# Kernel tuning notes

Hardware: AMD Instinct MI355X
Metric: run time of the kernel (lower is better)

Reference implementation:

```python
import jax, jax.numpy as jnp
import numpy as np

D = 512        # input_dim
T = 64         # n_trees
DEPTH = 3
NI = 2 ** DEPTH - 1   # 7 internal nodes
NL = 2 ** DEPTH       # 8 leaves
PPT = NI * D + NI + NL * 2   # params per tree
TOT = PPT * T + T            # + tree_weights
HID = 64


def setup_inputs() -> dict:
    key = jax.random.key(0)
    ks = jax.random.split(key, 10)
    w = lambda k, s: jax.random.normal(k, s, jnp.float32) * 0.05  # xavier-ish small gain
    return {
        "X_train": jax.random.normal(ks[0], (8192, D), jnp.float32),
        "X_test": jax.random.normal(ks[1], (32768, D), jnp.float32),
        "y_train": jax.random.randint(ks[2], (8192,), 0, 2, jnp.int64),
        "W1": w(ks[3], (HID, D)), "b1": jnp.zeros(HID), "g1": jnp.ones(HID), "be1": jnp.zeros(HID),
        "W2": w(ks[4], (HID, HID)), "b2": jnp.zeros(HID),
        "H1": w(ks[5], (2 * HID, HID)), "hb1": jnp.zeros(2 * HID),
        "g2": jnp.ones(2 * HID), "be2": jnp.zeros(2 * HID),
        "H2": w(ks[6], (2 * HID, 2 * HID)), "hb2": jnp.zeros(2 * HID),
        "H3": w(ks[7], (TOT, 2 * HID)), "hb3": jnp.zeros(TOT),
    }


def _ln(x, g, b, eps=1e-5):
    m = x.mean(-1, keepdims=True)
    v = ((x - m) ** 2).mean(-1, keepdims=True)
    return (x - m) / jnp.sqrt(v + eps) * g + b


def reference(X_train, X_test, y_train, W1, b1, g1, be1, W2, b2,
              H1, hb1, g2, be2, H2, hb2, H3, hb3):
    # --- hypernet: data encoder + param generator (Dropout is eval=identity) ---
    h = jax.nn.relu(_ln(X_train @ W1.T + b1, g1, be1))
    h = jax.nn.relu(h @ W2.T + b2)
    c = h.mean(axis=0)                              # [HID] context
    u = jax.nn.relu(_ln(c @ H1.T + hb1, g2, be2))
    u = jax.nn.relu(u @ H2.T + hb2)
    params = u @ H3.T + hb3                         # [TOT]

    # --- parse per-tree params (sequential layout) ---
    rows = params[: T * PPT].reshape(T, PPT)
    sw = rows[:, : NI * D].reshape(T, NI, D)        # split weights
    sb = rows[:, NI * D: NI * D + NI]               # split bias [T, NI]
    ll = rows[:, NI * D + NI:].reshape(T, NL, 2)    # leaf logits
    tw = params[T * PPT:]                           # tree weights [T]

    # --- soft decision trees, all trees/nodes batched ---
    # sigmoid split prob for every (sample, tree, internal node); temperature=1
    p = jax.nn.sigmoid(jnp.einsum('bd,tnd->btn', X_test, sw) + sb[None])  # [B,T,NI]
    B = X_test.shape[0]
    lp = jnp.ones((B, T, 1), X_test.dtype)
    for d in range(DEPTH):                          # unrolled fixed-depth traversal
        s = 2 ** d - 1                              # heap offset of level d
        pd = p[:, :, s: s + 2 ** d]                 # [B,T,2^d]
        lp = jnp.stack([lp * (1 - pd), lp * pd], axis=-1).reshape(B, T, 2 ** (d + 1))
    # original code adds leaf contributions twice (main loop + cleanup loop)
    lp = lp * 2.0                                   # [B,T,NL]

    leaf_dist = jax.nn.softmax(ll, axis=-1)         # [T,NL,2]
    out_t = jnp.einsum('btl,tlc->btc', lp, leaf_dist)
    w = jax.nn.softmax(tw, axis=0)                  # [T]
    return jnp.einsum('btc,t->bc', out_t, w)        # [B,2]
```

## Files before the change

kernel.cpp:

```cpp
#include <hip/hip_runtime.h>
#include <hip/hip_bf16.h>

#define DD 512
#define HIDN 64
#define NTREE 64
#define NIN 7
#define PPTC 3607
#define TOTP 230912
#define SWROWS 448

typedef __attribute__((ext_vector_type(8))) short bf16x8;
typedef __attribute__((ext_vector_type(4))) float f32x4;
typedef __attribute__((ext_vector_type(8))) _Float16 h16x8;

__device__ __forceinline__ unsigned short f2bf(float f) {
  unsigned u = __float_as_uint(f);
  unsigned r = (u + 0x7FFFu + ((u >> 16) & 1u)) >> 16;
  return (unsigned short)r;
}
__device__ __forceinline__ float sigmoidf_(float x) {
  return 1.0f / (1.0f + __expf(-x));
}
__device__ __forceinline__ uint2 pack_bf16x4(float4 v) {
  uint2 pk;
  pk.x = (unsigned)f2bf(v.x) | ((unsigned)f2bf(v.y) << 16);
  pk.y = (unsigned)f2bf(v.z) | ((unsigned)f2bf(v.w) << 16);
  return pk;
}
__device__ __forceinline__ bf16x8 cvt8(float4 a, float4 b) {
  unsigned u0, u1, u2, u3;
  asm("v_cvt_pk_bf16_f32 %0, %1, %2" : "=v"(u0) : "v"(a.x), "v"(a.y));
  asm("v_cvt_pk_bf16_f32 %0, %1, %2" : "=v"(u1) : "v"(a.z), "v"(a.w));
  asm("v_cvt_pk_bf16_f32 %0, %1, %2" : "=v"(u2) : "v"(b.x), "v"(b.y));
  asm("v_cvt_pk_bf16_f32 %0, %1, %2" : "=v"(u3) : "v"(b.z), "v"(b.w));
  union { unsigned u[4]; bf16x8 v; } r;
  r.u[0] = u0; r.u[1] = u1; r.u[2] = u2; r.u[3] = u3;
  return r.v;
}
__device__ __forceinline__ void gl_lds16(const void* g, void* l) {
  __builtin_amdgcn_global_load_lds(
      (const __attribute__((address_space(1))) unsigned int*)g,
      (__attribute__((address_space(3))) unsigned int*)l, 16, 0, 0);
}

__global__ __launch_bounds__(256) void k_train(
    const float* __restrict__ Xtr, const float* __restrict__ W1,
    const float* __restrict__ b1, const float* __restrict__ g1,
    const float* __restrict__ be1, const float* __restrict__ W2,
    const float* __restrict__ b2, float* __restrict__ c_part)
{
  __shared__ __align__(16) char smem[37888];
  char* Xc  = smem;
  char* W1c = smem + 8192;
  char* Hl  = smem + 24576;
  char* W2l = smem + 28672;
  float* lnb = (float*)(smem + 36864);
  float* cp  = (float*)(smem + 37376);

  const int tid = threadIdx.x;
  const int lane = tid & 63;
  const int wv = tid >> 6;
  const int l15 = lane & 15;
  const int gq = lane >> 4;
  const int wm = wv >> 1;
  const int wn = wv & 1;
  const int rb0 = blockIdx.x * 32;

  const float4* X4g = (const float4*)Xtr;
  const float4* W4g = (const float4*)W1;

#pragma unroll
  for (int s = 0; s < 4; ++s) {
    int fidx = tid + s * 256;
    int n = fidx >> 4, kq = fidx & 15;
    float4 v = ((const float4*)W2)[n * 16 + kq];
    uint2 pk = pack_bf16x4(v);
    int off = n * 128 + kq * 8; off ^= (n & 7) << 4;
    *(uint2*)(W2l + off) = pk;
  }

  int xga[4], xo[4];
#pragma unroll
  for (int s = 0; s < 4; ++s) {
    int f = tid + s * 256;
    int m = f >> 5, kq = f & 31;
    xga[s] = (rb0 + m) * 128 + kq;
    xo[s] = (m * 256 + kq * 8) ^ ((m & 7) << 4);
  }
  int wga[8], wo[8];
#pragma unroll
  for (int s = 0; s < 8; ++s) {
    int f = tid + s * 256;
    int n = f >> 5, kq = f & 31;
    wga[s] = n * 128 + kq;
    wo[s] = (n * 256 + kq * 8) ^ ((n & 7) << 4);
  }

  f32x4 acc1[2];
#pragma unroll
  for (int nt = 0; nt < 2; ++nt) { f32x4 z = {0.f,0.f,0.f,0.f}; acc1[nt] = z; }

  float4 xr[4], wr[8];
#pragma unroll
  for (int s = 0; s < 4; ++s) xr[s] = X4g[xga[s]];
#pragma unroll
  for (int s = 0; s < 8; ++s) wr[s] = W4g[wga[s]];

  for (int kc = 0; kc < 4; ++kc) {
    __syncthreads();
#pragma unroll
    for (int s = 0; s < 4; ++s) *(uint2*)(Xc + xo[s]) = pack_bf16x4(xr[s]);
#pragma unroll
    for (int s = 0; s < 8; ++s) *(uint2*)(W1c + wo[s]) = pack_bf16x4(wr[s]);
    if (kc < 3) {
      int ko = (kc + 1) * 32;
#pragma unroll
      for (int s = 0; s < 4; ++s) xr[s] = X4g[xga[s] + ko];
#pragma unroll
      for (int s = 0; s < 8; ++s) wr[s] = W4g[wga[s] + ko];
    }
    __syncthreads();
#pragma unroll
    for (int ks = 0; ks < 4; ++ks) {
      int arow = wm * 16 + l15;
      int aoff = (arow * 256 + ks * 64 + gq * 16) ^ ((arow & 7) << 4);
      bf16x8 afr = *(const bf16x8*)(Xc + aoff);
#pragma unroll
      for (int nt = 0; nt < 2; ++nt) {
        int brow = wn * 32 + nt * 16 + l15;
        int boff = (brow * 256 + ks * 64 + gq * 16) ^ ((brow & 7) << 4);
        bf16x8 bfr = *(const bf16x8*)(W1c + boff);
        acc1[nt] = __builtin_amdgcn_mfma_f32_16x16x32_bf16(afr, bfr, acc1[nt], 0, 0, 0);
      }
    }
  }

  float b1v[2], g1v[2], be1v[2], b2v[2];
#pragma unroll
  for (int nt = 0; nt < 2; ++nt) {
    int c = wn * 32 + nt * 16 + l15;
    b1v[nt] = b1[c]; g1v[nt] = g1[c]; be1v[nt] = be1[c]; b2v[nt] = b2[c];
  }
  float yv[2][4], s_[4], q_[4];
#pragma unroll
  for (int i = 0; i < 4; ++i) {
    float s = 0.f, q = 0.f;
#pragma unroll
    for (int nt = 0; nt < 2; ++nt) {
      float y = acc1[nt][i] + b1v[nt];
      yv[nt][i] = y; s += y; q += y * y;
    }
    s_[i] = s; q_[i] = q;
  }
#pragma unroll
  for (int off = 1; off < 16; off <<= 1) {
#pragma unroll
    for (int i = 0; i < 4; ++i) {
      s_[i] += __shfl_xor(s_[i], off);
      q_[i] += __shfl_xor(q_[i], off);
    }
  }
  if (l15 == 0) {
#pragma unroll
    for (int i = 0; i < 4; ++i) {
      int row = wm * 16 + gq * 4 + i;
      float2 sv; sv.x = s_[i]; sv.y = q_[i];
      *(float2*)(lnb + (row * 2 + wn) * 2) = sv;
    }
  }
  __syncthreads();
#pragma unroll
  for (int i = 0; i < 4; ++i) {
    int row = wm * 16 + gq * 4 + i;
    float2 e0 = *(float2*)(lnb + (row * 2 + 0) * 2);
    float2 e1 = *(float2*)(lnb + (row * 2 + 1) * 2);
    float m = (e0.x + e1.x) * (1.0f / 64.0f);
    float var = (e0.y + e1.y) * (1.0f / 64.0f) - m * m;
    float rstd = rsqrtf(var + 1e-5f);
#pragma unroll
    for (int nt = 0; nt < 2; ++nt) {
      float h = (yv[nt][i] - m) * rstd * g1v[nt] + be1v[nt];
      h = fmaxf(h, 0.0f);
      int col = wn * 32 + nt * 16 + l15;
      int off2 = (row * 128 + col * 2) ^ ((row & 7) << 4);
      *(unsigned short*)(Hl + off2) = f2bf(h);
    }
  }
  __syncthreads();

  f32x4 acc2[2];
#pragma unroll
  for (int nt = 0; nt < 2; ++nt) { f32x4 z = {0.f,0.f,0.f,0.f}; acc2[nt] = z; }
#pragma unroll
  for (int ks = 0; ks < 2; ++ks) {
    int arow = wm * 16 + l15;
    int aoff = (arow * 128 + ks * 64 + gq * 16) ^ ((arow & 7) << 4);
    bf16x8 afr = *(const bf16x8*)(Hl + aoff);
#pragma unroll
    for (int nt = 0; nt < 2; ++nt) {
      int brow = wn * 32 + nt * 16 + l15;
      int boff = (brow * 128 + ks * 64 + gq * 16) ^ ((brow & 7) << 4);
      bf16x8 bfr = *(const bf16x8*)(W2l + boff);
      acc2[nt] = __builtin_amdgcn_mfma_f32_16x16x32_bf16(afr, bfr, acc2[nt], 0, 0, 0);
    }
  }
  float cs[2];
#pragma unroll
  for (int nt = 0; nt < 2; ++nt) {
    float s = 0.f;
#pragma unroll
    for (int i = 0; i < 4; ++i) s += fmaxf(acc2[nt][i] + b2v[nt], 0.0f);
    cs[nt] = s;
  }
#pragma unroll
  for (int nt = 0; nt < 2; ++nt) {
    cs[nt] += __shfl_xor(cs[nt], 16);
    cs[nt] += __shfl_xor(cs[nt], 32);
  }
  if (lane < 16) {
#pragma unroll
    for (int nt = 0; nt < 2; ++nt)
      cp[wm * 64 + wn * 32 + nt * 16 + lane] = cs[nt];
  }
  __syncthreads();
  if (tid < 64) c_part[blockIdx.x * 64 + tid] = cp[tid] + cp[64 + tid];
}

__global__ __launch_bounds__(256) void k_head(
    const float* __restrict__ c_part,
    const float* __restrict__ H1, const float* __restrict__ hb1,
    const float* __restrict__ g2, const float* __restrict__ be2,
    const float* __restrict__ H2, const float* __restrict__ hb2,
    float* __restrict__ u2out)
{
  __shared__ float part[256];
  __shared__ float clds[64];
  __shared__ float u1lds[128];
  __shared__ float red[8];
  int tid = threadIdx.x;
  {
    int col = tid & 63, g = tid >> 6;
    float s0 = 0.f, s1 = 0.f, s2 = 0.f, s3 = 0.f;
    int b0 = g * 64;
    for (int b = 0; b < 64; b += 4) {
      s0 += c_part[(b0 + b + 0) * 64 + col];
      s1 += c_part[(b0 + b + 1) * 64 + col];
      s2 += c_part[(b0 + b + 2) * 64 + col];
      s3 += c_part[(b0 + b + 3) * 64 + col];
    }
    part[tid] = (s0 + s1) + (s2 + s3);
  }
  __syncthreads();
  if (tid < 64)
    clds[tid] = (part[tid] + part[64 + tid] + part[128 + tid] + part[192 + tid]) * (1.0f / 8192.0f);
  __syncthreads();
  float acc = 0.f;
  if (tid < 128) {
    float a0 = 0.f, a1 = 0.f, a2 = 0.f, a3 = 0.f;
    for (int k = 0; k < 64; k += 4) {
      a0 += clds[k + 0] * H1[tid * 64 + k + 0];
      a1 += clds[k + 1] * H1[tid * 64 + k + 1];
      a2 += clds[k + 2] * H1[tid * 64 + k + 2];
      a3 += clds[k + 3] * H1[tid * 64 + k + 3];
    }
    acc = hb1[tid] + ((a0 + a1) + (a2 + a3));
  }
  float s = acc, q = acc * acc;
#pragma unroll
  for (int off = 1; off < 64; off <<= 1) { s += __shfl_xor(s, off); q += __shfl_xor(q, off); }
  int wv = tid >> 6;
  if ((tid & 63) == 0) { red[wv * 2] = s; red[wv * 2 + 1] = q; }
  __syncthreads();
  float S = red[0] + red[2], Q = red[1] + red[3];
  float m = S * (1.0f / 128.0f);
  float var = Q * (1.0f / 128.0f) - m * m;
  float rstd = rsqrtf(var + 1e-5f);
  if (tid < 128)
    u1lds[tid] = fmaxf((acc - m) * rstd * g2[tid] + be2[tid], 0.0f);
  __syncthreads();
  if (tid < 128) {
    float c0 = 0.f, c1 = 0.f, c2 = 0.f, c3 = 0.f;
    for (int k = 0; k < 128; k += 4) {
      c0 += u1lds[k + 0] * H2[tid * 128 + k + 0];
      c1 += u1lds[k + 1] * H2[tid * 128 + k + 1];
      c2 += u1lds[k + 2] * H2[tid * 128 + k + 2];
      c3 += u1lds[k + 3] * H2[tid * 128 + k + 3];
    }
    u2out[tid] = fmaxf(hb2[tid] + ((c0 + c1) + (c2 + c3)), 0.0f);
  }
}

__global__ __launch_bounds__(256) void k_params(
    const float* __restrict__ H3, const float* __restrict__ hb3,
    const float* __restrict__ u2,
    unsigned short* __restrict__ Bsw, float* __restrict__ sb,
    float* __restrict__ ll, float* __restrict__ tw)
{
  __shared__ float u2l[128];
  int tid = threadIdx.x;
  if (tid < 128) u2l[tid] = u2[tid];
  __syncthreads();
  int row = blockIdx.x * 64 + (tid >> 2);
  int sub = tid & 3;
  float acc = 0.0f;
  const float4* H4 = (const float4*)H3;
#pragma unroll
  for (int j = 0; j < 8; ++j) {
    int f = j * 4 + sub;
    float4 v = H4[row * 32 + f];
    acc += v.x * u2l[f * 4] + v.y * u2l[f * 4 + 1] + v.z * u2l[f * 4 + 2] + v.w * u2l[f * 4 + 3];
  }
  acc += __shfl_xor(acc, 1);
  acc += __shfl_xor(acc, 2);
  if (sub == 0) {
    float val = acc + hb3[row];
    if (row >= 230848) {
      tw[row - 230848] = val;
    } else {
      int t = row / PPTC;
      int r = row - t * PPTC;
      if (r < 3584) {
        int n = r >> 9, d = r & 511;
        Bsw[(t * 7 + n) * 512 + d] = f2bf(val);
      } else if (r < 3591) {
        sb[t * 7 + (r - 3584)] = val;
      } else {
        ll[t * 16 + (r - 3591)] = val;
      }
    }
  }
}

__global__ __launch_bounds__(512) void k_test(
    const float* __restrict__ Xt, const unsigned short* __restrict__ Bsw,
    const float* __restrict__ sb, const float* __restrict__ ll,
    const float* __restrict__ tw, float* __restrict__ out)
{
  __shared__ __align__(16) char smem[154368];
  char* Pl = smem;
  float* qlds = (float*)(smem + 147456);
  float* sbl  = (float*)(smem + 151552);
  float* outl = (float*)(smem + 153344);

  const int tid = threadIdx.x;
  const int lane = tid & 63;
  const int wv = tid >> 6;
  const int l15 = lane & 15;
  const int gq = lane >> 4;
  const int wm = wv >> 2;
  const int wn = wv & 3;
  const int bm0 = blockIdx.x * 128;

  const float4* X4 = (const float4*)Xt;
  const uint4* B4 = (const uint4*)Bsw;

  if (tid < 448) sbl[tid] = sb[tid];
  if (tid < 64) {
    int t = tid;
    float x = tw[t];
    float m = x;
#pragma unroll
    for (int off = 1; off < 64; off <<= 1) m = fmaxf(m, __shfl_xor(m, off));
    float e = __expf(x - m);
    float s = e;
#pragma unroll
    for (int off = 1; off < 64; off <<= 1) s += __shfl_xor(s, off);
    float w = e / s;
#pragma unroll
    for (int l = 0; l < 8; ++l) {
      float a = ll[t * 16 + l * 2], b = ll[t * 16 + l * 2 + 1];
      float mm = fmaxf(a, b);
      float e0 = __expf(a - mm), e1 = __expf(b - mm);
      float inv = 2.0f * w / (e0 + e1);
      qlds[t * 16 + l * 2] = e0 * inv;
      qlds[t * 16 + l * 2 + 1] = e1 * inv;
    }
  }

  const int xkg0 = tid >> 7,         xrow0 = tid & 127;
  const int xkg1 = (tid + 512) >> 7, xrow1 = tid & 127;
#define ISSUE_TILE(t_) do { \
    char* xb_ = smem + ((t_) % 3) * 49152; \
    char* bb_ = xb_ + 16384; \
    gl_lds16(X4 + ((bm0 + xrow0) * 128 + (t_) * 8 + xkg0), xb_ + tid * 16); \
    gl_lds16(X4 + ((bm0 + xrow1) * 128 + (t_) * 8 + xkg1), xb_ + (tid + 512) * 16); \
    gl_lds16(B4 + (tid * 64 + (t_) * 4 + 0), bb_ + (0 * 512 + tid) * 16); \
    gl_lds16(B4 + (tid * 64 + (t_) * 4 + 1), bb_ + (1 * 512 + tid) * 16); \
    gl_lds16(B4 + (tid * 64 + (t_) * 4 + 2), bb_ + (2 * 512 + tid) * 16); \
    gl_lds16(B4 + (tid * 64 + (t_) * 4 + 3), bb_ + (3 * 512 + tid) * 16); \
  } while (0)

  f32x4 acc[4][7];
#pragma unroll
  for (int mt = 0; mt < 4; ++mt)
#pragma unroll
    for (int nt = 0; nt < 7; ++nt) { f32x4 z = {0.f,0.f,0.f,0.f}; acc[mt][nt] = z; }

#define COMPUTE_TILE(t_) do { \
    char* xb_ = smem + ((t_) % 3) * 49152; \
    char* bb_ = xb_ + 16384; \
    bf16x8 abf[4]; \
    _Pragma("unroll") \
    for (int mt = 0; mt < 4; ++mt) { \
      int row = wm * 64 + mt * 16 + l15; \
      float4 a0 = *(const float4*)(xb_ + ((2 * gq) * 128 + row) * 16); \
      float4 a1 = *(const float4*)(xb_ + ((2 * gq + 1) * 128 + row) * 16); \
      abf[mt] = cvt8(a0, a1); \
    } \
    _Pragma("unroll") \
    for (int nt = 0; nt < 7; ++nt) { \
      int n = wn * 112 + nt * 16 + l15; \
      bf16x8 bfr = *(const bf16x8*)(bb_ + (gq * 512 + n) * 16); \
      _Pragma("unroll") \
      for (int mt = 0; mt < 4; ++mt) \
        acc[mt][nt] = __builtin_amdgcn_mfma_f32_16x16x32_bf16(abf[mt], bfr, acc[mt][nt], 0, 0, 0); \
    } } while (0)

  ISSUE_TILE(0);
  ISSUE_TILE(1);
  ISSUE_TILE(2);

  for (int t = 0; t < 13; ++t) {
    asm volatile("s_waitcnt vmcnt(12)" ::: "memory");
    __builtin_amdgcn_sched_barrier(0);
    __builtin_amdgcn_s_barrier();
    COMPUTE_TILE(t);
    __builtin_amdgcn_s_barrier();
    ISSUE_TILE(t + 3);
  }
  asm volatile("s_waitcnt vmcnt(12)" ::: "memory");
  __builtin_amdgcn_sched_barrier(0);
  __builtin_amdgcn_s_barrier();
  COMPUTE_TILE(13);
  __builtin_amdgcn_s_barrier();
  asm volatile("s_waitcnt vmcnt(6)" ::: "memory");
  __builtin_amdgcn_sched_barrier(0);
  __builtin_amdgcn_s_barrier();
  COMPUTE_TILE(14);
  __builtin_amdgcn_s_barrier();
  asm volatile("s_waitcnt vmcnt(0)" ::: "memory");
  __builtin_amdgcn_sched_barrier(0);
  __builtin_amdgcn_s_barrier();
  COMPUTE_TILE(15);
  __syncthreads();

  float qreg[16];
  {
    const float4* q4 = (const float4*)qlds;
#pragma unroll
    for (int j = 0; j < 4; ++j) {
      float4 v = q4[lane * 4 + j];
      qreg[j * 4] = v.x; qreg[j * 4 + 1] = v.y; qreg[j * 4 + 2] = v.z; qreg[j * 4 + 3] = v.w;
    }
  }

#pragma unroll
  for (int rg = 0; rg < 4; ++rg) {
    if (wm == (rg >> 1)) {
#pragma unroll
      for (int mtl = 0; mtl < 2; ++mtl) {
        const int mt = (rg & 1) * 2 + mtl;
#pragma unroll
        for (int nt = 0; nt < 7; ++nt) {
          int col = wn * 112 + nt * 16 + l15;
          float sbv = sbl[col];
          int t = col / 7;
          int j = col - t * 7;
          int slot2 = (t * 8 + j) * 2;
#pragma unroll
          for (int i = 0; i < 4; ++i) {
            int rl = mtl * 16 + gq * 4 + i;
            float p = sigmoidf_(acc[mt][nt][i] + sbv);
            *(_Float16*)(Pl + rl * 1024 + slot2) = (_Float16)p;
          }
        }
      }
    }
    __syncthreads();
#pragma unroll
    for (int k = 0; k < 4; ++k) {
      int rl = wv * 4 + k;
      h16x8 v = *(const h16x8*)(Pl + rl * 1024 + lane * 16);
      float p0 = (float)v[0], p1 = (float)v[1], p2 = (float)v[2];
      float p3 = (float)v[3], p4 = (float)v[4], p5 = (float)v[5], p6 = (float)v[6];
      float n0 = 1.f - p0, n1 = 1.f - p1, n2 = 1.f - p2;
      float a00 = n0 * n1, a01 = n0 * p1, a10 = p0 * n2, a11 = p0 * p2;
      float L0 = a00 * (1.f - p3), L1 = a00 * p3;
      float L2 = a01 * (1.f - p4), L3 = a01 * p4;
      float L4 = a10 * (1.f - p5), L5 = a10 * p5;
      float L6 = a11 * (1.f - p6), L7 = a11 * p6;
      float o0 = L0*qreg[0] + L1*qreg[2] + L2*qreg[4] + L3*qreg[6]
               + L4*qreg[8] + L5*qreg[10] + L6*qreg[12] + L7*qreg[14];
      float o1 = L0*qreg[1] + L1*qreg[3] + L2*qreg[5] + L3*qreg[7]
               + L4*qreg[9] + L5*qreg[11] + L6*qreg[13] + L7*qreg[15];
#pragma unroll
      for (int off = 1; off < 64; off <<= 1) {
        o0 += __shfl_xor(o0, off);
        o1 += __shfl_xor(o1, off);
      }
      if (lane == 0) {
        int gr = rg * 32 + rl;
        outl[gr * 2] = o0;
        outl[gr * 2 + 1] = o1;
      }
    }
    __syncthreads();
  }
  if (tid < 256) out[bm0 * 2 + tid] = outl[tid];
#undef ISSUE_TILE
#undef COMPUTE_TILE
}

extern "C" void kernel_launch(void* const* d_in, const int* in_sizes, int n_in,
                              void* d_out, int out_size, void* d_ws, size_t ws_size,
                              hipStream_t stream)
{
  const float* Xtr = (const float*)d_in[0];
  const float* Xte = (const float*)d_in[1];
  const float* W1  = (const float*)d_in[3];
  const float* b1  = (const float*)d_in[4];
  const float* g1  = (const float*)d_in[5];
  const float* be1 = (const float*)d_in[6];
  const float* W2  = (const float*)d_in[7];
  const float* b2  = (const float*)d_in[8];
  const float* H1  = (const float*)d_in[9];
  const float* hb1 = (const float*)d_in[10];
  const float* g2  = (const float*)d_in[11];
  const float* be2 = (const float*)d_in[12];
  const float* H2  = (const float*)d_in[13];
  const float* hb2 = (const float*)d_in[14];
  const float* H3  = (const float*)d_in[15];
  const float* hb3 = (const float*)d_in[16];
  float* out = (float*)d_out;
  char* ws = (char*)d_ws;

  float* c_part = (float*)ws;
  float* u2     = (float*)(ws + 65536);
  float* sb     = (float*)(ws + 66048);
  float* ll     = (float*)(ws + 67840);
  float* tw     = (float*)(ws + 71936);
  unsigned short* Bsw = (unsigned short*)(ws + 72192);

  k_train<<<256, 256, 0, stream>>>(Xtr, W1, b1, g1, be1, W2, b2, c_part);
  k_head<<<1, 256, 0, stream>>>(c_part, H1, hb1, g2, be2, H2, hb2, u2);
  k_params<<<3608, 256, 0, stream>>>(H3, hb3, u2, Bsw, sb, ll, tw);
  k_test<<<256, 512, 0, stream>>>(Xte, Bsw, sb, ll, tw, out);
}
```

Before: 101.1 us.

## Pre-swizzle split weights into MFMA fragment layout and XOR-swizzle LDS tiles

The parameter kernel now writes bf16 split weights in a per-k-tile fragment layout with an XOR swizzle on the 8-element group index. This lets the test kernel load each B tile as one contiguous 32KB block and read fragments without LDS bank conflicts. The X tile staging moves to row-major order with an XOR-swizzled column group, and LDS addresses are precomputed outside the loop. The intent is to make global loads more coalesced and remove LDS bank conflicts. The cost is scattered bf16 stores in k_params and more complex indexing.

```diff
diff --git a/kernel.cpp b/kernel.cpp
--- a/kernel.cpp
+++ b/kernel.cpp
@@ -293,7 +293,7 @@
 __global__ __launch_bounds__(256) void k_params(
     const float* __restrict__ H3, const float* __restrict__ hb3,
     const float* __restrict__ u2,
-    unsigned short* __restrict__ Bsw, float* __restrict__ sb,
+    unsigned short* __restrict__ Bfrag, float* __restrict__ sb,
     float* __restrict__ ll, float* __restrict__ tw)
 {
   __shared__ float u2l[128];
@@ -321,7 +321,9 @@
       int r = row - t * PPTC;
       if (r < 3584) {
         int n = r >> 9, d = r & 511;
-        Bsw[(t * 7 + n) * 512 + d] = f2bf(val);
+        int col = t * 7 + n;
+        int kt = d >> 5, gq = (d >> 3) & 3, j = d & 7;
+        Bfrag[kt * 16384 + col * 32 + (gq ^ (col & 3)) * 8 + j] = f2bf(val);
       } else if (r < 3591) {
         sb[t * 7 + (r - 3584)] = val;
       } else {
@@ -332,7 +334,7 @@
 }
 
 __global__ __launch_bounds__(512) void k_test(
-    const float* __restrict__ Xt, const unsigned short* __restrict__ Bsw,
+    const float* __restrict__ Xt, const unsigned short* __restrict__ Bfrag,
     const float* __restrict__ sb, const float* __restrict__ ll,
     const float* __restrict__ tw, float* __restrict__ out)
 {
@@ -352,7 +354,7 @@
   const int bm0 = blockIdx.x * 128;
 
   const float4* X4 = (const float4*)Xt;
-  const uint4* B4 = (const uint4*)Bsw;
+  const char* Bf = (const char*)Bfrag;
 
   if (tid < 448) sbl[tid] = sb[tid];
   if (tid < 64) {
@@ -377,17 +379,21 @@
     }
   }
 
-  const int xkg0 = tid >> 7,         xrow0 = tid & 127;
-  const int xkg1 = (tid + 512) >> 7, xrow1 = tid & 127;
+  const int xrow0 = tid >> 3;
+  const int xpg   = (tid & 7) ^ (xrow0 & 7);
+  const int xsrc0 = (bm0 + xrow0) * 128 + xpg;
+  const int xsrc1 = (bm0 + xrow0 + 64) * 128 + xpg;
+
 #define ISSUE_TILE(t_) do { \
     char* xb_ = smem + ((t_) % 3) * 49152; \
     char* bb_ = xb_ + 16384; \
-    gl_lds16(X4 + ((bm0 + xrow0) * 128 + (t_) * 8 + xkg0), xb_ + tid * 16); \
-    gl_lds16(X4 + ((bm0 + xrow1) * 128 + (t_) * 8 + xkg1), xb_ + (tid + 512) * 16); \
-    gl_lds16(B4 + (tid * 64 + (t_) * 4 + 0), bb_ + (0 * 512 + tid) * 16); \
-    gl_lds16(B4 + (tid * 64 + (t_) * 4 + 1), bb_ + (1 * 512 + tid) * 16); \
-    gl_lds16(B4 + (tid * 64 + (t_) * 4 + 2), bb_ + (2 * 512 + tid) * 16); \
-    gl_lds16(B4 + (tid * 64 + (t_) * 4 + 3), bb_ + (3 * 512 + tid) * 16); \
+    gl_lds16(X4 + (xsrc0 + (t_) * 8), xb_ + tid * 16); \
+    gl_lds16(X4 + (xsrc1 + (t_) * 8), xb_ + (tid + 512) * 16); \
+    const char* bt_ = Bf + (t_) * 32768; \
+    gl_lds16(bt_ + tid * 16,          bb_ + tid * 16); \
+    gl_lds16(bt_ + (tid + 512) * 16,  bb_ + (tid + 512) * 16); \
+    gl_lds16(bt_ + (tid + 1024) * 16, bb_ + (tid + 1024) * 16); \
+    gl_lds16(bt_ + (tid + 1536) * 16, bb_ + (tid + 1536) * 16); \
   } while (0)
 
   f32x4 acc[4][7];
@@ -395,6 +401,16 @@
   for (int mt = 0; mt < 4; ++mt)
 #pragma unroll
     for (int nt = 0; nt < 7; ++nt) { f32x4 z = {0.f,0.f,0.f,0.f}; acc[mt][nt] = z; }
+
+  const int xoff0 = (((gq * 2) ^ (l15 & 7)) << 4);
+  const int xoff1 = (((gq * 2 + 1) ^ (l15 & 7)) << 4);
+  int arow[4];
+#pragma unroll
+  for (int mt = 0; mt < 4; ++mt) arow[mt] = (wm * 64 + mt * 16 + l15) * 128;
+  const int bxor = ((gq ^ (l15 & 3)) << 4);
+  int boffs[7];
+#pragma unroll
+  for (int nt = 0; nt < 7; ++nt) boffs[nt] = (wn * 112 + nt * 16 + l15) * 64 + bxor;
 
 #define COMPUTE_TILE(t_) do { \
     char* xb_ = smem + ((t_) % 3) * 49152; \
@@ -402,15 +418,13 @@
     bf16x8 abf[4]; \
     _Pragma("unroll") \
     for (int mt = 0; mt < 4; ++mt) { \
-      int row = wm * 64 + mt * 16 + l15; \
-      float4 a0 = *(const float4*)(xb_ + ((2 * gq) * 128 + row) * 16); \
-      float4 a1 = *(const float4*)(xb_ + ((2 * gq + 1) * 128 + row) * 16); \
+      float4 a0 = *(const float4*)(xb_ + arow[mt] + xoff0); \
+      float4 a1 = *(const float4*)(xb_ + arow[mt] + xoff1); \
       abf[mt] = cvt8(a0, a1); \
     } \
     _Pragma("unroll") \
     for (int nt = 0; nt < 7; ++nt) { \
-      int n = wn * 112 + nt * 16 + l15; \
-      bf16x8 bfr = *(const bf16x8*)(bb_ + (gq * 512 + n) * 16); \
+      bf16x8 bfr = *(const bf16x8*)(bb_ + boffs[nt]); \
       _Pragma("unroll") \
       for (int mt = 0; mt < 4; ++mt) \
         acc[mt][nt] = __builtin_amdgcn_mfma_f32_16x16x32_bf16(abf[mt], bfr, acc[mt][nt], 0, 0, 0); \
@@ -419,6 +433,7 @@
   ISSUE_TILE(0);
   ISSUE_TILE(1);
   ISSUE_TILE(2);
+  asm volatile("s_waitcnt lgkmcnt(0)" ::: "memory");
 
   for (int t = 0; t < 13; ++t) {
     asm volatile("s_waitcnt vmcnt(12)" ::: "memory");
@@ -539,10 +554,10 @@
   float* sb     = (float*)(ws + 66048);
   float* ll     = (float*)(ws + 67840);
   float* tw     = (float*)(ws + 71936);
-  unsigned short* Bsw = (unsigned short*)(ws + 72192);
+  unsigned short* Bfrag = (unsigned short*)(ws + 72192);
 
   k_train<<<256, 256, 0, stream>>>(Xtr, W1, b1, g1, be1, W2, b2, c_part);
   k_head<<<1, 256, 0, stream>>>(c_part, H1, hb1, g2, be2, H2, hb2, u2);
-  k_params<<<3608, 256, 0, stream>>>(H3, hb3, u2, Bsw, sb, ll, tw);
-  k_test<<<256, 512, 0, stream>>>(Xte, Bsw, sb, ll, tw, out);
-}
+  k_params<<<3608, 256, 0, stream>>>(H3, hb3, u2, Bfrag, sb, ll, tw);
+  k_test<<<256, 512, 0, stream>>>(Xte, Bfrag, sb, ll, tw, out);
+}
```

Measured after the change: 84.53 us. 1.2x faster.
